# Optimization experiments

Hardware: AMD Instinct MI355X
Metric: run time of the kernel (lower is better)

## Reference

```python
import jax, jax.numpy as jnp
import numpy as np


def _leaky(x):
    return jnp.where(x >= 0, x, 0.01 * x)  # nn.LeakyReLU default slope


def _conv1x1(x, w):
    # x: [B, C, H, W], w: [O, C] (1x1 conv == per-pixel channel GEMM)
    return jnp.einsum('bchw,oc->bohw', x, w)


def setup_inputs() -> dict:
    key = jax.random.key(0)
    ks = jax.random.split(key, 12)

    def kaiming(k, o, c):  # kaiming_normal_ fan_out, relu gain, 1x1 kernel
        return jax.random.normal(k, (o, c), jnp.float32) * np.float32(np.sqrt(2.0 / o))

    lr_feature = jax.random.normal(ks[0], (1, 32, 256, 512), jnp.float32)
    hr_feature = jax.random.normal(ks[1], (1, 32, 512, 1024), jnp.float32)
    return {
        'lr_feature': lr_feature,
        'hr_feature': hr_feature,
        's1_w0': kaiming(ks[2], 128, 128),
        's1_w1': kaiming(ks[3], 64, 128),
        's1_w2': kaiming(ks[4], 32, 64),
        's1_w3': kaiming(ks[5], 16, 32),
        's1_w4': kaiming(ks[6], 8, 16),
        's1_w5': kaiming(ks[7], 1, 8),
        's2_w0': kaiming(ks[8], 3, 3),
        's2_w1': kaiming(ks[9], 2, 3),
        's2_w2': kaiming(ks[10], 1, 2),
        'fuse_w': jnp.ones((1, 2), jnp.float32),  # fuse weight initialized to 1
    }


def reference(lr_feature, hr_feature, s1_w0, s1_w1, s1_w2, s1_w3, s1_w4, s1_w5,
              s2_w0, s2_w1, s2_w2, fuse_w):
    scale = hr_feature.shape[-1] // lr_feature.shape[-1]  # static python int (=2, even)
    Hh, Wh = hr_feature.shape[-2], hr_feature.shape[-1]

    # nearest-neighbor upsample of lr_feature by `scale` (expand/view trick in torch)
    lr_up = jnp.repeat(jnp.repeat(lr_feature, scale, axis=2), scale, axis=3)

    # representation: [B, 128, Hh, Wh]
    rep = jnp.concatenate(
        [lr_up, hr_feature, lr_up * hr_feature, (lr_up - hr_feature) ** 2], axis=1)

    # similarity_measure1: 1x1-conv MLP chain 128->128->64->32->16->8->1
    o = _leaky(_conv1x1(rep, s1_w0))
    o = _leaky(_conv1x1(o, s1_w1))
    o = _leaky(_conv1x1(o, s1_w2))
    o = _leaky(_conv1x1(o, s1_w3))
    o = _conv1x1(o, s1_w4)
    weights1 = _conv1x1(o, s1_w5)  # [B, 1, Hh, Wh]

    # distance matrix (even-scale branch): 3 channels [dx, dy, norm]
    v = jnp.arange(-(scale // 2), scale // 2 + 1, dtype=jnp.float32)
    m = v.shape[0] // 2
    v = jnp.concatenate([v[:m], v[m + 1:]])  # drop center -> length `scale`
    d0 = jnp.broadcast_to(v[None, :], (scale, scale))
    dm = jnp.stack([d0, d0.T, jnp.sqrt(d0 ** 2 + d0.T ** 2)], axis=0)  # [3,s,s]
    dm = jnp.tile(dm, (1, Hh // scale, Wh // scale))[None]  # [1, 3, Hh, Wh]

    # similarity_measure2: 3->3->2->1
    w2 = _leaky(_conv1x1(dm, s2_w0))
    w2 = _leaky(_conv1x1(w2, s2_w1))
    weights2 = _conv1x1(w2, s2_w2)  # [1, 1, Hh, Wh]

    # fuse (weight forced non-negative via abs, as in forward's .data mutation)
    mapping = _conv1x1(jnp.concatenate([weights1, weights2], axis=1), jnp.abs(fuse_w))
    return mapping
```

## Files before the change

### kernel.cpp

```cpp
#include <hip/hip_runtime.h>

typedef short v8s __attribute__((ext_vector_type(8)));
typedef float v4f __attribute__((ext_vector_type(4)));
typedef unsigned v4u __attribute__((ext_vector_type(4)));

#define Wh   1024
#define Hh   512
#define HWh  (Wh * Hh)
#define Wlr  512
#define HWlr (Wlr * 256)
#define ITERS 8
#define NBLK  512

#define WFRAG_SHORTS (53 * 512)
#define LDS_BYTES    (WFRAG_SHORTS * 2)

__device__ __forceinline__ unsigned short f2bf(float f) {
    union { float f; unsigned u; } v; v.f = f;
    unsigned r = v.u + 0x7FFFu + ((v.u >> 16) & 1u);
    return (unsigned short)(r >> 16);
}
__device__ __forceinline__ unsigned pk2(float a, float b) {
    union { float f; unsigned u; } ua, ub;
    ua.f = a; ub.f = b;
    return __builtin_amdgcn_perm(ub.u + 0x8000u, ua.u + 0x8000u, 0x07060302u);
}
__device__ __forceinline__ float leaky(float x) { return fmaxf(x, 0.01f * x); }

__device__ __forceinline__ v8s relay(v4f e, v4f o) {
    v4u w;
    w[0] = pk2(leaky(e[0]), leaky(e[1]));
    w[1] = pk2(leaky(e[2]), leaky(e[3]));
    w[2] = pk2(leaky(o[0]), leaky(o[1]));
    w[3] = pk2(leaky(o[2]), leaky(o[3]));
    return __builtin_bit_cast(v8s, w);
}

__global__ __launch_bounds__(512, 2)
void cmfsm_kernel(const float* __restrict__ lr, const float* __restrict__ hr,
                  const float* __restrict__ w0g, const float* __restrict__ w1g,
                  const float* __restrict__ w2g, const float* __restrict__ w3g,
                  const float* __restrict__ w4g, const float* __restrict__ w5g,
                  const float* __restrict__ t0g, const float* __restrict__ t1g,
                  const float* __restrict__ t2g, const float* __restrict__ fwg,
                  float* __restrict__ out)
{
    extern __shared__ unsigned short smem[];
    unsigned short* wfrag = smem;

    const int tid  = threadIdx.x;
    const int lane = tid & 63;
    const int wv   = tid >> 6;
    const int p    = lane & 15;
    const int q    = lane >> 4;

    for (int e = tid; e < 32 * 64; e += 512) {
        int f = e >> 6, l = e & 63;
        int mt = f >> 2, ks = f & 3, pp = l & 15, qq = l >> 4;
        const float* src = w0g + (mt * 16 + pp) * 128 + ks * 32 + qq * 8;
        unsigned short* dst = wfrag + f * 512 + l * 8;
#pragma unroll
        for (int j = 0; j < 8; ++j) dst[j] = f2bf(src[j]);
    }
    for (int e = tid; e < 16 * 64; e += 512) {
        int f = e >> 6, l = e & 63;
        int mt = f >> 2, ks = f & 3, pp = l & 15, qq = l >> 4;
        const float* srcrow = w1g + (mt * 16 + pp) * 128;
        unsigned short* dst = wfrag + (32 + f) * 512 + l * 8;
#pragma unroll
        for (int j = 0; j < 8; ++j)
            dst[j] = f2bf(srcrow[ks * 32 + ((j >> 2) << 4) + qq * 4 + (j & 3)]);
    }
    if (tid < 4 * 64) {
        int f = tid >> 6, l = tid & 63;
        int mt = f >> 1, ks = f & 1, pp = l & 15, qq = l >> 4;
        const float* srcrow = w2g + (mt * 16 + pp) * 64;
        unsigned short* dst = wfrag + (48 + f) * 512 + l * 8;
#pragma unroll
        for (int j = 0; j < 8; ++j)
            dst[j] = f2bf(srcrow[ks * 32 + ((j >> 2) << 4) + qq * 4 + (j & 3)]);
    }
    if (tid < 64) {
        int l = tid;
        int pp = l & 15, qq = l >> 4;
        const float* srcrow = w3g + pp * 32;
        unsigned short* dst = wfrag + 52 * 512 + l * 8;
#pragma unroll
        for (int j = 0; j < 8; ++j)
            dst[j] = f2bf(srcrow[((j >> 2) << 4) + qq * 4 + (j & 3)]);
    }

    float w45[4];
#pragma unroll
    for (int r = 0; r < 4; ++r) {
        float s = 0.f;
#pragma unroll
        for (int j = 0; j < 8; ++j) s += w5g[j] * w4g[j * 16 + q * 4 + r];
        w45[r] = s;
    }

    float w2e, w2o;
    {
        float tab[4];
#pragma unroll
        for (int yp = 0; yp < 2; ++yp)
#pragma unroll
            for (int xp = 0; xp < 2; ++xp) {
                float i0 = xp ? 1.f : -1.f;
                float i1 = yp ? 1.f : -1.f;
                float i2 = 1.41421356237309505f;
                float h0[3], h1[2];
                for (int o = 0; o < 3; ++o)
                    h0[o] = leaky(t0g[o*3+0]*i0 + t0g[o*3+1]*i1 + t0g[o*3+2]*i2);
                for (int o = 0; o < 2; ++o)
                    h1[o] = leaky(t1g[o*3+0]*h0[0] + t1g[o*3+1]*h0[1] + t1g[o*3+2]*h0[2]);
                tab[yp*2+xp] = t2g[0]*h1[0] + t2g[1]*h1[1];
            }
        const int yp = blockIdx.x & 1;
        w2e = yp ? tab[2] : tab[0];
        w2o = yp ? tab[3] : tab[1];
    }
    const float fa = fabsf(fwg[0]);
    const float fb = fabsf(fwg[1]);

    __syncthreads();

    const unsigned short* WL = wfrag + lane * 8;

    const float* hrp[8];
    const float* lrp[8];
    {
        const int hbase = blockIdx.x * Wh + wv * 16 + p;
        const int lbase = (blockIdx.x >> 1) * Wlr + wv * 8 + (p >> 1);
#pragma unroll
        for (int j = 0; j < 8; ++j) {
            hrp[j] = hr + (size_t)(q * 8 + j) * HWh  + hbase;
            lrp[j] = lr + (size_t)(q * 8 + j) * HWlr + lbase;
        }
    }

    const v8s a3 = *(const v8s*)(WL + 52 * 512);

    const int obase = blockIdx.x * Wh + wv * 16 + p;

    float h[8], l[8];
#pragma unroll
    for (int j = 0; j < 8; ++j) { h[j] = hrp[j][0]; l[j] = lrp[j][0]; }

#pragma unroll
    for (int it = 0; it < ITERS; ++it) {
        v4u bf0, bf1, bf2, bf3;
#pragma unroll
        for (int u = 0; u < 4; ++u) {
            float l0 = l[2*u], l1 = l[2*u+1];
            float h0 = h[2*u], h1 = h[2*u+1];
            bf0[u] = pk2(l0, l1);
            bf1[u] = pk2(h0, h1);
            bf2[u] = pk2(l0 * h0, l1 * h1);
            float d0 = l0 - h0, d1 = l1 - h1;
            bf3[u] = pk2(d0 * d0, d1 * d1);
        }
        v8s b0 = __builtin_bit_cast(v8s, bf0);
        v8s b1 = __builtin_bit_cast(v8s, bf1);
        v8s b2 = __builtin_bit_cast(v8s, bf2);
        v8s b3 = __builtin_bit_cast(v8s, bf3);

        if (it + 1 < ITERS) {
            const int ho = (it + 1) * 128;
            const int lo = (it + 1) * 64;
#pragma unroll
            for (int j = 0; j < 8; ++j) {
                h[j] = hrp[j][ho];
                l[j] = lrp[j][lo];
            }
        }

        v8s c1[4];
#pragma unroll
        for (int ksp = 0; ksp < 4; ++ksp) {
            v4f ae = (v4f){0.f, 0.f, 0.f, 0.f};
            v4f ao = (v4f){0.f, 0.f, 0.f, 0.f};
#pragma unroll
            for (int ks = 0; ks < 4; ++ks) {
                v8s b = (ks == 0) ? b0 : (ks == 1) ? b1 : (ks == 2) ? b2 : b3;
                v8s we = *(const v8s*)(WL + ((2 * ksp)     * 4 + ks) * 512);
                v8s wo = *(const v8s*)(WL + ((2 * ksp + 1) * 4 + ks) * 512);
                ae = __builtin_amdgcn_mfma_f32_16x16x32_bf16(we, b, ae, 0, 0, 0);
                ao = __builtin_amdgcn_mfma_f32_16x16x32_bf16(wo, b, ao, 0, 0, 0);
            }
            c1[ksp] = relay(ae, ao);
        }

        v8s c2[2];
#pragma unroll
        for (int ksp = 0; ksp < 2; ++ksp) {
            v4f ae = (v4f){0.f, 0.f, 0.f, 0.f};
            v4f ao = (v4f){0.f, 0.f, 0.f, 0.f};
#pragma unroll
            for (int ks = 0; ks < 4; ++ks) {
                v8s we = *(const v8s*)(WL + (32 + (2 * ksp)     * 4 + ks) * 512);
                v8s wo = *(const v8s*)(WL + (32 + (2 * ksp + 1) * 4 + ks) * 512);
                ae = __builtin_amdgcn_mfma_f32_16x16x32_bf16(we, c1[ks], ae, 0, 0, 0);
                ao = __builtin_amdgcn_mfma_f32_16x16x32_bf16(wo, c1[ks], ao, 0, 0, 0);
            }
            c2[ksp] = relay(ae, ao);
        }

        v8s c3;
        {
            v4f ae = (v4f){0.f, 0.f, 0.f, 0.f};
            v4f ao = (v4f){0.f, 0.f, 0.f, 0.f};
#pragma unroll
            for (int ks = 0; ks < 2; ++ks) {
                v8s we = *(const v8s*)(WL + (48 +     ks) * 512);
                v8s wo = *(const v8s*)(WL + (48 + 2 + ks) * 512);
                ae = __builtin_amdgcn_mfma_f32_16x16x32_bf16(we, c2[ks], ae, 0, 0, 0);
                ao = __builtin_amdgcn_mfma_f32_16x16x32_bf16(wo, c2[ks], ao, 0, 0, 0);
            }
            c3 = relay(ae, ao);
        }

        {
            v4f acc3 = __builtin_amdgcn_mfma_f32_16x16x32_bf16(a3, c3, (v4f){0.f, 0.f, 0.f, 0.f}, 0, 0, 0);

            float part = 0.f;
#pragma unroll
            for (int r = 0; r < 4; ++r) part += w45[r] * leaky(acc3[r]);
            part += __shfl_xor(part, 16, 64);
            part += __shfl_xor(part, 32, 64);

            if (q == 0) {
                const float w2v = (p & 1) ? w2o : w2e;
                out[obase + it * 128] = fa * part + fb * w2v;
            }
        }
    }
}

extern "C" void kernel_launch(void* const* d_in, const int* in_sizes, int n_in,
                              void* d_out, int out_size, void* d_ws, size_t ws_size,
                              hipStream_t stream) {
    const float* lr  = (const float*)d_in[0];
    const float* hr  = (const float*)d_in[1];
    const float* w0g = (const float*)d_in[2];
    const float* w1g = (const float*)d_in[3];
    const float* w2g = (const float*)d_in[4];
    const float* w3g = (const float*)d_in[5];
    const float* w4g = (const float*)d_in[6];
    const float* w5g = (const float*)d_in[7];
    const float* t0g = (const float*)d_in[8];
    const float* t1g = (const float*)d_in[9];
    const float* t2g = (const float*)d_in[10];
    const float* fwg = (const float*)d_in[11];
    float* out = (float*)d_out;

    hipLaunchKernelGGL(cmfsm_kernel, dim3(NBLK), dim3(512), LDS_BYTES, stream,
                       lr, hr, w0g, w1g, w2g, w3g, w4g, w5g, t0g, t1g, t2g, fwg, out);
}
```

Measured before the change: 148.5 us.

## Split rows across two blocks, raise occupancy, use hardware bf16 pack

Doubles the grid so each block covers half an output row with half the iterations, and raises the launch-bounds occupancy hint from 2 to 6 blocks per CU to expose more parallelism and latency hiding. Replaces the manual add-and-permute bf16 packing with the native v_cvt_pk_bf16_f32 instruction. Peels the first MFMA of each chain so it accumulates into a shared zero vector. Each block still stages the full weight fragment set in LDS, so weight-staging overhead doubles, and the higher occupancy target may force register spills or leave LDS as the real occupancy limit.

```diff
diff --git a/kernel.cpp b/kernel.cpp
--- a/kernel.cpp
+++ b/kernel.cpp
@@ -9,8 +9,8 @@
 #define HWh  (Wh * Hh)
 #define Wlr  512
 #define HWlr (Wlr * 256)
-#define ITERS 8
-#define NBLK  512
+#define ITERS 4
+#define NBLK  1024
 
 #define WFRAG_SHORTS (53 * 512)
 #define LDS_BYTES    (WFRAG_SHORTS * 2)
@@ -21,9 +21,9 @@
     return (unsigned short)(r >> 16);
 }
 __device__ __forceinline__ unsigned pk2(float a, float b) {
-    union { float f; unsigned u; } ua, ub;
-    ua.f = a; ub.f = b;
-    return __builtin_amdgcn_perm(ub.u + 0x8000u, ua.u + 0x8000u, 0x07060302u);
+    unsigned r;
+    asm("v_cvt_pk_bf16_f32 %0, %1, %2" : "=v"(r) : "v"(a), "v"(b));
+    return r;
 }
 __device__ __forceinline__ float leaky(float x) { return fmaxf(x, 0.01f * x); }
 
@@ -36,7 +36,7 @@
     return __builtin_bit_cast(v8s, w);
 }
 
-__global__ __launch_bounds__(512, 2)
+__global__ __launch_bounds__(512, 6)
 void cmfsm_kernel(const float* __restrict__ lr, const float* __restrict__ hr,
                   const float* __restrict__ w0g, const float* __restrict__ w1g,
                   const float* __restrict__ w2g, const float* __restrict__ w3g,
@@ -99,6 +99,9 @@
         w45[r] = s;
     }
 
+    const int row  = blockIdx.x >> 1;
+    const int half = blockIdx.x & 1;
+
     float w2e, w2o;
     {
         float tab[4];
@@ -116,7 +119,7 @@
                     h1[o] = leaky(t1g[o*3+0]*h0[0] + t1g[o*3+1]*h0[1] + t1g[o*3+2]*h0[2]);
                 tab[yp*2+xp] = t2g[0]*h1[0] + t2g[1]*h1[1];
             }
-        const int yp = blockIdx.x & 1;
+        const int yp = row & 1;
         w2e = yp ? tab[2] : tab[0];
         w2o = yp ? tab[3] : tab[1];
     }
@@ -130,8 +133,8 @@
     const float* hrp[8];
     const float* lrp[8];
     {
-        const int hbase = blockIdx.x * Wh + wv * 16 + p;
-        const int lbase = (blockIdx.x >> 1) * Wlr + wv * 8 + (p >> 1);
+        const int hbase = row * Wh + half * 512 + wv * 16 + p;
+        const int lbase = (row >> 1) * Wlr + half * 256 + wv * 8 + (p >> 1);
 #pragma unroll
         for (int j = 0; j < 8; ++j) {
             hrp[j] = hr + (size_t)(q * 8 + j) * HWh  + hbase;
@@ -141,7 +144,9 @@
 
     const v8s a3 = *(const v8s*)(WL + 52 * 512);
 
-    const int obase = blockIdx.x * Wh + wv * 16 + p;
+    const v4f z4 = (v4f){0.f, 0.f, 0.f, 0.f};
+
+    const int obase = row * Wh + half * 512 + wv * 16 + p;
 
     float h[8], l[8];
 #pragma unroll
@@ -178,11 +183,13 @@
         v8s c1[4];
 #pragma unroll
         for (int ksp = 0; ksp < 4; ++ksp) {
-            v4f ae = (v4f){0.f, 0.f, 0.f, 0.f};
-            v4f ao = (v4f){0.f, 0.f, 0.f, 0.f};
-#pragma unroll
-            for (int ks = 0; ks < 4; ++ks) {
-                v8s b = (ks == 0) ? b0 : (ks == 1) ? b1 : (ks == 2) ? b2 : b3;
+            v4f ae = __builtin_amdgcn_mfma_f32_16x16x32_bf16(
+                         *(const v8s*)(WL + ((2 * ksp)     * 4) * 512), b0, z4, 0, 0, 0);
+            v4f ao = __builtin_amdgcn_mfma_f32_16x16x32_bf16(
+                         *(const v8s*)(WL + ((2 * ksp + 1) * 4) * 512), b0, z4, 0, 0, 0);
+#pragma unroll
+            for (int ks = 1; ks < 4; ++ks) {
+                v8s b = (ks == 1) ? b1 : (ks == 2) ? b2 : b3;
                 v8s we = *(const v8s*)(WL + ((2 * ksp)     * 4 + ks) * 512);
                 v8s wo = *(const v8s*)(WL + ((2 * ksp + 1) * 4 + ks) * 512);
                 ae = __builtin_amdgcn_mfma_f32_16x16x32_bf16(we, b, ae, 0, 0, 0);
@@ -194,10 +201,12 @@
         v8s c2[2];
 #pragma unroll
         for (int ksp = 0; ksp < 2; ++ksp) {
-            v4f ae = (v4f){0.f, 0.f, 0.f, 0.f};
-            v4f ao = (v4f){0.f, 0.f, 0.f, 0.f};
-#pragma unroll
-            for (int ks = 0; ks < 4; ++ks) {
+            v4f ae = __builtin_amdgcn_mfma_f32_16x16x32_bf16(
+                         *(const v8s*)(WL + (32 + (2 * ksp)     * 4) * 512), c1[0], z4, 0, 0, 0);
+            v4f ao = __builtin_amdgcn_mfma_f32_16x16x32_bf16(
+                         *(const v8s*)(WL + (32 + (2 * ksp + 1) * 4) * 512), c1[0], z4, 0, 0, 0);
+#pragma unroll
+            for (int ks = 1; ks < 4; ++ks) {
                 v8s we = *(const v8s*)(WL + (32 + (2 * ksp)     * 4 + ks) * 512);
                 v8s wo = *(const v8s*)(WL + (32 + (2 * ksp + 1) * 4 + ks) * 512);
                 ae = __builtin_amdgcn_mfma_f32_16x16x32_bf16(we, c1[ks], ae, 0, 0, 0);
@@ -208,20 +217,19 @@
 
         v8s c3;
         {
-            v4f ae = (v4f){0.f, 0.f, 0.f, 0.f};
-            v4f ao = (v4f){0.f, 0.f, 0.f, 0.f};
-#pragma unroll
-            for (int ks = 0; ks < 2; ++ks) {
-                v8s we = *(const v8s*)(WL + (48 +     ks) * 512);
-                v8s wo = *(const v8s*)(WL + (48 + 2 + ks) * 512);
-                ae = __builtin_amdgcn_mfma_f32_16x16x32_bf16(we, c2[ks], ae, 0, 0, 0);
-                ao = __builtin_amdgcn_mfma_f32_16x16x32_bf16(wo, c2[ks], ao, 0, 0, 0);
-            }
+            v4f ae = __builtin_amdgcn_mfma_f32_16x16x32_bf16(
+                         *(const v8s*)(WL + 48 * 512), c2[0], z4, 0, 0, 0);
+            v4f ao = __builtin_amdgcn_mfma_f32_16x16x32_bf16(
+                         *(const v8s*)(WL + 50 * 512), c2[0], z4, 0, 0, 0);
+            ae = __builtin_amdgcn_mfma_f32_16x16x32_bf16(
+                     *(const v8s*)(WL + 49 * 512), c2[1], ae, 0, 0, 0);
+            ao = __builtin_amdgcn_mfma_f32_16x16x32_bf16(
+                     *(const v8s*)(WL + 51 * 512), c2[1], ao, 0, 0, 0);
             c3 = relay(ae, ao);
         }
 
         {
-            v4f acc3 = __builtin_amdgcn_mfma_f32_16x16x32_bf16(a3, c3, (v4f){0.f, 0.f, 0.f, 0.f}, 0, 0, 0);
+            v4f acc3 = __builtin_amdgcn_mfma_f32_16x16x32_bf16(a3, c3, z4, 0, 0, 0);
 
             float part = 0.f;
 #pragma unroll
```

Measured after the change: 189.5 us. +27.6%, slower.
